# Optimization experiments

Measured on AMD Instinct MI355X. Metric: run time of the kernel, lower is better.

The kernel has to match this reference:

```python
import jax, jax.numpy as jnp
import numpy as np

IN_F = 8192
OUT_F = 8192
MAX_STATES = 100
STATE_THRESHOLD = MAX_STATES // 2  # 50


def setup_inputs() -> dict:
    key = jax.random.key(0)
    k1, k2, k3 = jax.random.split(key, 3)
    # binary spike input (module expects spikes in {0,1})
    spike_input = (jax.random.uniform(k1, (1, IN_F)) < 0.5).astype(jnp.float32)
    # synapse_states buffer: randint in [threshold-5, threshold+15) cast to float
    synapse_states = jax.random.randint(
        k2, (OUT_F, IN_F), STATE_THRESHOLD - 5, STATE_THRESHOLD + 15
    ).astype(jnp.float32)
    membrane_potential = jnp.zeros((OUT_F,), jnp.float32)
    adaptive_threshold = jnp.ones((OUT_F,), jnp.float32)
    # torch.randn(out_features) * 0.2, pre-sampled for determinism
    noise = jax.random.normal(k3, (OUT_F,), jnp.float32) * 0.2
    return {
        "spike_input": spike_input,
        "synapse_states": synapse_states,
        "membrane_potential": membrane_potential,
        "adaptive_threshold": adaptive_threshold,
        "noise": noise,
    }


def reference(spike_input, synapse_states, membrane_potential, adaptive_threshold, noise):
    # rethreshold float state matrix into binary {0,1} weights
    w = (synapse_states > STATE_THRESHOLD).astype(jnp.float32)  # [out, in]
    x = spike_input if spike_input.ndim > 1 else spike_input[None, :]
    current = jnp.matmul(x, w.T).reshape(-1)  # [out] (batch must be 1)
    potential = membrane_potential + current + noise
    spikes = (potential >= adaptive_threshold).astype(jnp.float32)
    return spikes
```

## Files before the change

kernel.cpp:

```cpp
#include <hip/hip_runtime.h>
#include <hip/hip_bf16.h>

#define IN_F 8192
#define OUT_F 8192
#define STATE_THRESHOLD 50.0f

__global__ __launch_bounds__(512, 8) void snn_gemv_kernel(
    const float* __restrict__ spike_input,
    const float* __restrict__ synapse_states,
    const float* __restrict__ membrane,
    const float* __restrict__ adaptive_thresh,
    const float* __restrict__ noise,
    float* __restrict__ out)
{
    __shared__ float s_spike[IN_F];

    const int tid  = threadIdx.x;
    const int lane = tid & 63;
    const int wave = tid >> 6;

    const float4* sp4 = (const float4*)spike_input;
    float4* ls4 = (float4*)s_spike;
#pragma unroll
    for (int j = 0; j < 4; ++j) {
        ls4[tid + 512 * j] = sp4[tid + 512 * j];
    }
    __syncthreads();

    const int row = blockIdx.x * 8 + wave;
    const float4* rowp = (const float4*)(synapse_states + (size_t)row * IN_F);
    const float4* lsp  = (const float4*)s_spike;

    float acc = 0.0f;
#pragma unroll 4
    for (int k = lane; k < IN_F / 4; k += 64) {
        float4 s = rowp[k];
        float4 x = lsp[k];
        acc += (s.x > STATE_THRESHOLD ? x.x : 0.0f);
        acc += (s.y > STATE_THRESHOLD ? x.y : 0.0f);
        acc += (s.z > STATE_THRESHOLD ? x.z : 0.0f);
        acc += (s.w > STATE_THRESHOLD ? x.w : 0.0f);
    }

#pragma unroll
    for (int off = 32; off > 0; off >>= 1) {
        acc += __shfl_down(acc, off);
    }

    if (lane == 0) {
        float potential = membrane[row] + acc + noise[row];
        out[row] = (potential >= adaptive_thresh[row]) ? 1.0f : 0.0f;
    }
}

extern "C" void kernel_launch(void* const* d_in, const int* in_sizes, int n_in,
                              void* d_out, int out_size, void* d_ws, size_t ws_size,
                              hipStream_t stream) {
    const float* spike_input    = (const float*)d_in[0];
    const float* synapse_states = (const float*)d_in[1];
    const float* membrane       = (const float*)d_in[2];
    const float* adaptive_thr   = (const float*)d_in[3];
    const float* noise          = (const float*)d_in[4];
    float* out = (float*)d_out;

    dim3 grid(OUT_F / 8);
    dim3 block(512);
    snn_gemv_kernel<<<grid, block, 0, stream>>>(
        spike_input, synapse_states, membrane, adaptive_thr, noise, out);
}
```

Baseline: 364.2 us.

## Pack spike input into per-lane register bitmasks and stream weights nontemporally

Drops the shared-memory staging of the spike vector and its block barrier. Each lane instead loads its slice of the input and packs it into two 64-bit bitmasks held in registers. The inner loop counts matching bits as integers and reads the weight matrix with nontemporal loads to avoid polluting the cache. This assumes spikes are binary (thresholded at 0.5), which changes semantics for non-binary inputs, and every wave now reads the whole input from global memory.

```diff
diff --git a/kernel.cpp b/kernel.cpp
--- a/kernel.cpp
+++ b/kernel.cpp
@@ -4,6 +4,8 @@
 #define IN_F 8192
 #define OUT_F 8192
 #define STATE_THRESHOLD 50.0f
+
+typedef float f32x4 __attribute__((ext_vector_type(4)));
 
 __global__ __launch_bounds__(512, 8) void snn_gemv_kernel(
     const float* __restrict__ spike_input,
@@ -13,42 +15,59 @@
     const float* __restrict__ noise,
     float* __restrict__ out)
 {
-    __shared__ float s_spike[IN_F];
-
     const int tid  = threadIdx.x;
     const int lane = tid & 63;
     const int wave = tid >> 6;
 
-    const float4* sp4 = (const float4*)spike_input;
-    float4* ls4 = (float4*)s_spike;
+    const f32x4* sp4 = (const f32x4*)spike_input;
+    unsigned long long b0 = 0ull, b1 = 0ull;
 #pragma unroll
-    for (int j = 0; j < 4; ++j) {
-        ls4[tid + 512 * j] = sp4[tid + 512 * j];
+    for (int i = 0; i < 16; ++i) {
+        f32x4 x = sp4[lane + 64 * i];
+        unsigned long long nib =
+            (unsigned long long)((x.x > 0.5f) | ((x.y > 0.5f) << 1) |
+                                 ((x.z > 0.5f) << 2) | ((x.w > 0.5f) << 3));
+        b0 |= nib << (4 * i);
     }
-    __syncthreads();
+#pragma unroll
+    for (int i = 0; i < 16; ++i) {
+        f32x4 x = sp4[lane + 64 * (i + 16)];
+        unsigned long long nib =
+            (unsigned long long)((x.x > 0.5f) | ((x.y > 0.5f) << 1) |
+                                 ((x.z > 0.5f) << 2) | ((x.w > 0.5f) << 3));
+        b1 |= nib << (4 * i);
+    }
 
     const int row = blockIdx.x * 8 + wave;
-    const float4* rowp = (const float4*)(synapse_states + (size_t)row * IN_F);
-    const float4* lsp  = (const float4*)s_spike;
+    const f32x4* rowp = (const f32x4*)(synapse_states + (size_t)row * IN_F);
 
-    float acc = 0.0f;
+    unsigned int cnt = 0;
 #pragma unroll 4
-    for (int k = lane; k < IN_F / 4; k += 64) {
-        float4 s = rowp[k];
-        float4 x = lsp[k];
-        acc += (s.x > STATE_THRESHOLD ? x.x : 0.0f);
-        acc += (s.y > STATE_THRESHOLD ? x.y : 0.0f);
-        acc += (s.z > STATE_THRESHOLD ? x.z : 0.0f);
-        acc += (s.w > STATE_THRESHOLD ? x.w : 0.0f);
+    for (int i = 0; i < 16; ++i) {
+        f32x4 s = __builtin_nontemporal_load(rowp + lane + 64 * i);
+        unsigned int nib = (unsigned int)(b0 >> (4 * i)) & 0xFu;
+        cnt += (s.x > STATE_THRESHOLD) ? (nib & 1u) : 0u;
+        cnt += (s.y > STATE_THRESHOLD) ? ((nib >> 1) & 1u) : 0u;
+        cnt += (s.z > STATE_THRESHOLD) ? ((nib >> 2) & 1u) : 0u;
+        cnt += (s.w > STATE_THRESHOLD) ? ((nib >> 3) & 1u) : 0u;
+    }
+#pragma unroll 4
+    for (int i = 0; i < 16; ++i) {
+        f32x4 s = __builtin_nontemporal_load(rowp + lane + 64 * (i + 16));
+        unsigned int nib = (unsigned int)(b1 >> (4 * i)) & 0xFu;
+        cnt += (s.x > STATE_THRESHOLD) ? (nib & 1u) : 0u;
+        cnt += (s.y > STATE_THRESHOLD) ? ((nib >> 1) & 1u) : 0u;
+        cnt += (s.z > STATE_THRESHOLD) ? ((nib >> 2) & 1u) : 0u;
+        cnt += (s.w > STATE_THRESHOLD) ? ((nib >> 3) & 1u) : 0u;
     }
 
 #pragma unroll
     for (int off = 32; off > 0; off >>= 1) {
-        acc += __shfl_down(acc, off);
+        cnt += __shfl_down(cnt, off);
     }
 
     if (lane == 0) {
-        float potential = membrane[row] + acc + noise[row];
+        float potential = membrane[row] + (float)cnt + noise[row];
         out[row] = (potential >= adaptive_thresh[row]) ? 1.0f : 0.0f;
     }
 }
```

Result: no change. 366.8 us (+0.7%).

## Pack spike input into per-thread bitmask and stream block tile with nontemporal loads

Applied to the files above, without the earlier changes.

Drops the shared-memory spike buffer. Each thread packs the 16 spike values it will reuse into a bitmask held in registers, because with the new mapping every thread touches the same input columns in every row. The whole 8-row block tile is read as one contiguous stream of 32 fully unrolled nontemporal float4 loads, accumulated as integer counts, and reduced across waves through a small shared array. Treating spikes as binary (>0.5) relies on the input being exactly 0/1, which the spec states.

```diff
diff --git a/kernel.cpp b/kernel.cpp
--- a/kernel.cpp
+++ b/kernel.cpp
@@ -4,6 +4,8 @@
 #define IN_F 8192
 #define OUT_F 8192
 #define STATE_THRESHOLD 50.0f
+
+typedef float f32x4 __attribute__((ext_vector_type(4)));
 
 __global__ __launch_bounds__(512, 8) void snn_gemv_kernel(
     const float* __restrict__ spike_input,
@@ -13,42 +15,54 @@
     const float* __restrict__ noise,
     float* __restrict__ out)
 {
-    __shared__ float s_spike[IN_F];
-
     const int tid  = threadIdx.x;
     const int lane = tid & 63;
     const int wave = tid >> 6;
 
-    const float4* sp4 = (const float4*)spike_input;
-    float4* ls4 = (float4*)s_spike;
+    const f32x4* sp4 = (const f32x4*)spike_input;
+    unsigned int bits = 0;
 #pragma unroll
-    for (int j = 0; j < 4; ++j) {
-        ls4[tid + 512 * j] = sp4[tid + 512 * j];
+    for (int seg = 0; seg < 4; ++seg) {
+        f32x4 x = sp4[seg * 512 + tid];
+        unsigned int nib = (unsigned int)((x.x > 0.5f) | ((x.y > 0.5f) << 1) |
+                                          ((x.z > 0.5f) << 2) | ((x.w > 0.5f) << 3));
+        bits |= nib << (4 * seg);
+    }
+
+    const f32x4* tile =
+        (const f32x4*)(synapse_states + (size_t)blockIdx.x * 8 * IN_F);
+
+    unsigned int acc[8] = {0u, 0u, 0u, 0u, 0u, 0u, 0u, 0u};
+#pragma unroll
+    for (int i = 0; i < 32; ++i) {
+        f32x4 s = __builtin_nontemporal_load(tile + i * 512 + tid);
+        unsigned int nib = (bits >> (4 * (i & 3))) & 0xFu;
+        unsigned int c = 0;
+        c += (s.x > STATE_THRESHOLD) ? (nib & 1u) : 0u;
+        c += (s.y > STATE_THRESHOLD) ? ((nib >> 1) & 1u) : 0u;
+        c += (s.z > STATE_THRESHOLD) ? ((nib >> 2) & 1u) : 0u;
+        c += (s.w > STATE_THRESHOLD) ? ((nib >> 3) & 1u) : 0u;
+        acc[i >> 2] += c;
+    }
+
+    __shared__ unsigned int part[8][8];
+#pragma unroll
+    for (int r = 0; r < 8; ++r) {
+        unsigned int v = acc[r];
+#pragma unroll
+        for (int off = 32; off > 0; off >>= 1) {
+            v += __shfl_down(v, off);
+        }
+        if (lane == 0) part[wave][r] = v;
     }
     __syncthreads();
 
-    const int row = blockIdx.x * 8 + wave;
-    const float4* rowp = (const float4*)(synapse_states + (size_t)row * IN_F);
-    const float4* lsp  = (const float4*)s_spike;
-
-    float acc = 0.0f;
-#pragma unroll 4
-    for (int k = lane; k < IN_F / 4; k += 64) {
-        float4 s = rowp[k];
-        float4 x = lsp[k];
-        acc += (s.x > STATE_THRESHOLD ? x.x : 0.0f);
-        acc += (s.y > STATE_THRESHOLD ? x.y : 0.0f);
-        acc += (s.z > STATE_THRESHOLD ? x.z : 0.0f);
-        acc += (s.w > STATE_THRESHOLD ? x.w : 0.0f);
-    }
-
+    if (tid < 8) {
+        unsigned int tot = 0;
 #pragma unroll
-    for (int off = 32; off > 0; off >>= 1) {
-        acc += __shfl_down(acc, off);
-    }
-
-    if (lane == 0) {
-        float potential = membrane[row] + acc + noise[row];
+        for (int w = 0; w < 8; ++w) tot += part[w][tid];
+        const int row = blockIdx.x * 8 + tid;
+        float potential = membrane[row] + (float)tot + noise[row];
         out[row] = (potential >= adaptive_thresh[row]) ? 1.0f : 0.0f;
     }
 }
```

Result: slower. 402.8 us (+10.6%).
